# Optimization experiments

Measured on AMD Instinct MI355X. Metric: run time of the kernel, lower is better.

The kernel has to match this reference:

```python
import jax, jax.numpy as jnp
import numpy as np

B, E, T, N = 1024, 512, 8, 256


def setup_inputs() -> dict:
    key = jax.random.key(0)
    k1, k2, k3, k4 = jax.random.split(key, 4)
    weights = jax.random.uniform(k1, (T,), dtype=jnp.float32)  # one scalar per bond type
    bond_src = jax.random.randint(k2, (B, E), 0, N - 1, dtype=jnp.int32)  # raw i, offset +1 later
    bond_dst = jax.random.randint(k3, (B, E), 0, N - 1, dtype=jnp.int32)
    bond_type = jax.random.randint(k4, (B, E), 0, T, dtype=jnp.int32)
    return {"weights": weights, "bond_src": bond_src, "bond_dst": bond_dst,
            "bond_type": bond_type, "num_nodes": N}


def reference(weights, bond_src, bond_dst, bond_type, num_nodes):
    # Gather per-bond weight, then symmetric scatter into dense [B, N, N] adjacency.
    batch, n_edges = bond_src.shape
    w = weights[bond_type]                                  # [B, E] gather
    bidx = jnp.broadcast_to(jnp.arange(batch)[:, None], (batch, n_edges))
    src = bond_src + 1                                      # +1 node offset as in torch code
    dst = bond_dst + 1
    bond_matrix = jnp.zeros((batch, num_nodes, num_nodes), dtype=weights.dtype)
    bond_matrix = bond_matrix.at[bidx, src, dst].set(w)
    bond_matrix = bond_matrix.at[bidx, dst, src].set(w)
    return bond_matrix
```

## Files before the change

kernel.cpp:

```cpp
#include <hip/hip_runtime.h>


#define NB_E 512
#define NB_N 256
#define CH_ROWS 64
#define CH_WORDS (CH_ROWS * NB_N / 2)

typedef float v4f __attribute__((ext_vector_type(4)));

__device__ __forceinline__ void lds_max_u16(unsigned int* tab, int cell, unsigned int v16)
{
    unsigned int* w = tab + (cell >> 1);
    const int sh = (cell & 1) * 16;
    unsigned int old = *w;
    while (true) {
        const unsigned int cur = (old >> sh) & 0xFFFFu;
        if (cur >= v16) break;
        const unsigned int nw = (old & ~(0xFFFFu << sh)) | (v16 << sh);
        const unsigned int seen = atomicCAS(w, old, nw);
        if (seen == old) break;
        old = seen;
    }
}

__global__ __launch_bounds__(256) void BondWeight_41738492182540_kernel(
    const float* __restrict__ weights,
    const int*   __restrict__ bsrc,
    const int*   __restrict__ bdst,
    const int*   __restrict__ btyp,
    float*       __restrict__ out)
{
    __shared__ unsigned int seqtab[CH_WORDS];
    __shared__ float s_wt[8];

    const int bx = blockIdx.x;
    const int b  = bx >> 2;
    const int r0 = (bx & 3) * CH_ROWS;
    const int t  = threadIdx.x;

    if (t < 8) s_wt[t] = weights[t];

    {
        uint4* tab4 = (uint4*)seqtab;
        #pragma unroll
        for (int k = 0; k < CH_WORDS / 4 / 256; ++k)
            tab4[t + 256 * k] = make_uint4(0u, 0u, 0u, 0u);
    }

    const int2 s2 = ((const int2*)(bsrc + b * NB_E))[t];
    const int2 d2 = ((const int2*)(bdst + b * NB_E))[t];
    const int2 y2 = ((const int2*)(btyp + b * NB_E))[t];

    int row[4], col[4];
    unsigned int pk[4];
    {
        const int e0 = 2 * t, e1 = 2 * t + 1;
        const int sa = s2.x + 1, da = d2.x + 1;
        const int sb = s2.y + 1, db = d2.y + 1;
        const unsigned int ta = (unsigned int)y2.x & 7u;
        const unsigned int tb = (unsigned int)y2.y & 7u;
        row[0] = sa; col[0] = da; pk[0] = ((unsigned int)(e0 + 1) << 3) | ta;
        row[1] = sb; col[1] = db; pk[1] = ((unsigned int)(e1 + 1) << 3) | tb;
        row[2] = da; col[2] = sa; pk[2] = ((unsigned int)(NB_E + e0 + 1) << 3) | ta;
        row[3] = db; col[3] = sb; pk[3] = ((unsigned int)(NB_E + e1 + 1) << 3) | tb;
    }

    __syncthreads();

    #pragma unroll
    for (int i = 0; i < 4; ++i) {
        const int r = row[i] - r0;
        if (0 <= r && r < CH_ROWS)
            lds_max_u16(seqtab, r * NB_N + col[i], pk[i]);
    }

    __syncthreads();

    float4* __restrict__ out4 = ((float4*)out)
        + (size_t)b * (NB_N * NB_N / 4) + r0 * (NB_N / 4);
    const uint2* __restrict__ tab2 = (const uint2*)seqtab;

    #pragma unroll
    for (int k = 0; k < (CH_ROWS * NB_N / 4) / 256; ++k) {
        const int i4 = t + 256 * k;
        const uint2 ab = tab2[i4];
        v4f v;
        unsigned int p;
        p = ab.x & 0xFFFFu; v.x = p ? s_wt[p & 7u] : 0.0f;
        p = ab.x >> 16;     v.y = p ? s_wt[p & 7u] : 0.0f;
        p = ab.y & 0xFFFFu; v.z = p ? s_wt[p & 7u] : 0.0f;
        p = ab.y >> 16;     v.w = p ? s_wt[p & 7u] : 0.0f;
        *(v4f*)&out4[i4] = v;
    }
}

extern "C" void kernel_launch(void* const* d_in, const int* in_sizes, int n_in,
                              void* d_out, int out_size, void* d_ws, size_t ws_size,
                              hipStream_t stream) {
    const float* weights = (const float*)d_in[0];
    const int*   bsrc    = (const int*)d_in[1];
    const int*   bdst    = (const int*)d_in[2];
    const int*   btyp    = (const int*)d_in[3];
    float*       out     = (float*)d_out;

    const int nb = in_sizes[1] / NB_E;

    BondWeight_41738492182540_kernel<<<nb * 4, 256, 0, stream>>>(
        weights, bsrc, bdst, btyp, out);
}
```

Measured before the change: 275.5 us.

## Split rows finer and stage resolved float weights in LDS before streaming out

Each block now handles 32 rows instead of 64, doubling the grid to eight blocks per batch. After the LDS max-resolution pass, the winning edges write their float weight into a second LDS float table, and the output loop becomes a plain vector copy from LDS with no per-element decode. This removes the per-cell branch and the s_wt lookups from the store loop, at the cost of zeroing an extra 32 KB LDS table, adding one more barrier, and re-reading the edge lists twice as often.

```diff
diff --git a/kernel.cpp b/kernel.cpp
--- a/kernel.cpp
+++ b/kernel.cpp
@@ -3,8 +3,9 @@
 
 #define NB_E 512
 #define NB_N 256
-#define CH_ROWS 64
-#define CH_WORDS (CH_ROWS * NB_N / 2)
+#define CH_ROWS 32
+#define SEQ_WORDS (CH_ROWS * NB_N / 2)
+#define W_FLOATS  (CH_ROWS * NB_N)
 
 typedef float v4f __attribute__((ext_vector_type(4)));
 
@@ -30,67 +31,84 @@
     const int*   __restrict__ btyp,
     float*       __restrict__ out)
 {
-    __shared__ unsigned int seqtab[CH_WORDS];
-    __shared__ float s_wt[8];
+    __shared__ unsigned int seqtab[SEQ_WORDS];
+    __shared__ float        wtab[W_FLOATS];
 
     const int bx = blockIdx.x;
-    const int b  = bx >> 2;
-    const int r0 = (bx & 3) * CH_ROWS;
+    const int b  = bx >> 3;
+    const int r0 = (bx & 7) * CH_ROWS;
     const int t  = threadIdx.x;
 
-    if (t < 8) s_wt[t] = weights[t];
-
     {
-        uint4* tab4 = (uint4*)seqtab;
+        uint4* s4 = (uint4*)seqtab;
         #pragma unroll
-        for (int k = 0; k < CH_WORDS / 4 / 256; ++k)
-            tab4[t + 256 * k] = make_uint4(0u, 0u, 0u, 0u);
+        for (int k = 0; k < SEQ_WORDS / 4 / 256; ++k)
+            s4[t + 256 * k] = make_uint4(0u, 0u, 0u, 0u);
+        float4* w4 = (float4*)wtab;
+        const float4 fz = make_float4(0.f, 0.f, 0.f, 0.f);
+        #pragma unroll
+        for (int k = 0; k < W_FLOATS / 4 / 256; ++k)
+            w4[t + 256 * k] = fz;
     }
 
     const int2 s2 = ((const int2*)(bsrc + b * NB_E))[t];
     const int2 d2 = ((const int2*)(bdst + b * NB_E))[t];
     const int2 y2 = ((const int2*)(btyp + b * NB_E))[t];
+    const float wA = weights[y2.x & 7];
+    const float wB = weights[y2.y & 7];
 
-    int row[4], col[4];
-    unsigned int pk[4];
+    int cell[4]; unsigned int pk[4]; float wv[4]; bool inw[4];
     {
         const int e0 = 2 * t, e1 = 2 * t + 1;
         const int sa = s2.x + 1, da = d2.x + 1;
         const int sb = s2.y + 1, db = d2.y + 1;
         const unsigned int ta = (unsigned int)y2.x & 7u;
         const unsigned int tb = (unsigned int)y2.y & 7u;
-        row[0] = sa; col[0] = da; pk[0] = ((unsigned int)(e0 + 1) << 3) | ta;
-        row[1] = sb; col[1] = db; pk[1] = ((unsigned int)(e1 + 1) << 3) | tb;
-        row[2] = da; col[2] = sa; pk[2] = ((unsigned int)(NB_E + e0 + 1) << 3) | ta;
-        row[3] = db; col[3] = sb; pk[3] = ((unsigned int)(NB_E + e1 + 1) << 3) | tb;
+        const int rr[4] = { sa, sb, da, db };
+        const int cc[4] = { da, db, sa, sb };
+        const unsigned int qq[4] = {
+            ((unsigned int)(e0 + 1) << 3) | ta,
+            ((unsigned int)(e1 + 1) << 3) | tb,
+            ((unsigned int)(NB_E + e0 + 1) << 3) | ta,
+            ((unsigned int)(NB_E + e1 + 1) << 3) | tb };
+        const float ww[4] = { wA, wB, wA, wB };
+        #pragma unroll
+        for (int i = 0; i < 4; ++i) {
+            const int r = rr[i] - r0;
+            inw[i]  = (0 <= r) && (r < CH_ROWS);
+            cell[i] = r * NB_N + cc[i];
+            pk[i]   = qq[i];
+            wv[i]   = ww[i];
+        }
     }
 
     __syncthreads();
 
     #pragma unroll
+    for (int i = 0; i < 4; ++i)
+        if (inw[i]) lds_max_u16(seqtab, cell[i], pk[i]);
+
+    __syncthreads();
+
+    #pragma unroll
     for (int i = 0; i < 4; ++i) {
-        const int r = row[i] - r0;
-        if (0 <= r && r < CH_ROWS)
-            lds_max_u16(seqtab, r * NB_N + col[i], pk[i]);
+        if (inw[i]) {
+            const unsigned int w32 = seqtab[cell[i] >> 1];
+            const unsigned int cur = (w32 >> ((cell[i] & 1) * 16)) & 0xFFFFu;
+            if (cur == pk[i]) wtab[cell[i]] = wv[i];
+        }
     }
 
     __syncthreads();
 
-    float4* __restrict__ out4 = ((float4*)out)
+    v4f* __restrict__ out4 = ((v4f*)out)
         + (size_t)b * (NB_N * NB_N / 4) + r0 * (NB_N / 4);
-    const uint2* __restrict__ tab2 = (const uint2*)seqtab;
+    const v4f* __restrict__ w4 = (const v4f*)wtab;
 
     #pragma unroll
-    for (int k = 0; k < (CH_ROWS * NB_N / 4) / 256; ++k) {
+    for (int k = 0; k < W_FLOATS / 4 / 256; ++k) {
         const int i4 = t + 256 * k;
-        const uint2 ab = tab2[i4];
-        v4f v;
-        unsigned int p;
-        p = ab.x & 0xFFFFu; v.x = p ? s_wt[p & 7u] : 0.0f;
-        p = ab.x >> 16;     v.y = p ? s_wt[p & 7u] : 0.0f;
-        p = ab.y & 0xFFFFu; v.z = p ? s_wt[p & 7u] : 0.0f;
-        p = ab.y >> 16;     v.w = p ? s_wt[p & 7u] : 0.0f;
-        *(v4f*)&out4[i4] = v;
+        out4[i4] = w4[i4];
     }
 }
 
@@ -105,6 +123,6 @@
 
     const int nb = in_sizes[1] / NB_E;
 
-    BondWeight_41738492182540_kernel<<<nb * 4, 256, 0, stream>>>(
+    BondWeight_41738492182540_kernel<<<nb * 8, 256, 0, stream>>>(
         weights, bsrc, bdst, btyp, out);
 }
```

Result: no change. 279.9 us (+1.6%).
